# Optimization experiments

Measured on AMD Instinct MI355X. Metric: run time of the kernel, lower is better.

Reference implementation:

```python
import jax, jax.numpy as jnp
import numpy as np

EPS = 1e-12  # tf.linalg.l2_normalize epsilon

def l2norm(x, axis):
    sq = jnp.sum(x * x, axis=axis, keepdims=True)
    return x * jax.lax.rsqrt(jnp.maximum(sq, EPS))

def setup_inputs() -> dict:
    key = jax.random.key(0)
    k1, k2, k3, k4 = jax.random.split(key, 4)
    B, S, D = 32, 2048, 1024
    X = jax.random.normal(k1, (B, S, D), dtype=jnp.float32)
    lengths = jax.random.randint(k2, (B,), 1, S + 1).astype(jnp.int32)
    W_global = jax.random.normal(k3, (D, D), dtype=jnp.float32) / np.sqrt(D)
    W_local = jax.random.normal(k4, (D, D), dtype=jnp.float32) / np.sqrt(D)
    return {"X": X, "lengths": lengths, "W_global": W_global, "W_local": W_local}

def reference(X, lengths, W_global, W_local):
    B, S, D = X.shape
    # ragged -> dense with mask: token s valid iff s < lengths[b]
    mask = (jnp.arange(S)[None, :] < lengths[:, None]).astype(X.dtype)  # [B,S]
    Xm = X * mask[:, :, None]
    # global projection of sequence-sum, l2-normalized per example
    gp = l2norm(jnp.sum(Xm, axis=1) @ W_global, axis=1)  # [B,D]
    # per-token local projection, l2-normalized per token
    lp = l2norm(jnp.einsum('bsd,de->bse', Xm, W_local), axis=2)  # [B,S,D]
    # dot-product attention of local projections against global vector
    attention = jnp.einsum('bsd,bd->bs', lp, gp) * mask  # [B,S]
    # attention-weighted sum over the (ragged) sequence
    return jnp.einsum('bs,bsd->bd', attention, Xm)  # [B,D]
```

## Files before the change

### kernel.cpp

```cpp
#include <hip/hip_runtime.h>

#define NB 32
#define NS 2048
#define ND 1024

typedef unsigned short u16;
typedef unsigned int u32;
typedef __attribute__((ext_vector_type(8))) short bf16x8;
typedef __attribute__((ext_vector_type(4))) float f32x4;

__device__ __forceinline__ u16 f2bf(float f) {
    u32 u = __float_as_uint(f);
    u32 r = u + 0x7fffu + ((u >> 16) & 1u);
    return (u16)(r >> 16);
}
__device__ __forceinline__ float bf2f(u32 lo16) {
    return __uint_as_float(lo16 << 16);
}
__device__ __forceinline__ void gload_lds16(const void* g, void* l) {
    __builtin_amdgcn_global_load_lds((const __attribute__((address_space(1))) void*)g,
                                     (__attribute__((address_space(3))) void*)l, 16, 0, 0);
}

template <bool DO_STASH>
__global__ void k_prep(const float* __restrict__ X, const int* __restrict__ len,
                       float* __restrict__ sumX, u16* __restrict__ stash) {
    int b = blockIdx.x >> 5, c = blockIdx.x & 31;
    int L = len[b];
    int s0 = c * 64;
    if (s0 >= L) return;
    int n = min(64, L - s0);
    int t = threadIdx.x;
    const float4* base = (const float4*)(X + (size_t)b * NS * ND + (size_t)s0 * ND) + t;
    char* img = (char*)stash + ((size_t)blockIdx.x << 17);
    float4 acc = {0.f, 0.f, 0.f, 0.f};
    for (int i = 0; i < n; ++i) {
        float4 x = base[i * (ND / 4)];
        acc.x += x.x; acc.y += x.y; acc.z += x.z; acc.w += x.w;
        if constexpr (DO_STASH) {
            u32 lo = (u32)f2bf(x.x) | ((u32)f2bf(x.y) << 16);
            u32 hi = (u32)f2bf(x.z) | ((u32)f2bf(x.w) << 16);
            u32 off = (u32)i * 2048u + (((u32)t * 8u) ^ (((u32)(i & 7)) << 4));
            *(uint2*)(img + off) = make_uint2(lo, hi);
        }
    }
    if constexpr (DO_STASH) {
        for (int i = n; i < 64; ++i) {
            u32 off = (u32)i * 2048u + (((u32)t * 8u) ^ (((u32)(i & 7)) << 4));
            *(uint2*)(img + off) = make_uint2(0u, 0u);
        }
    }
    float* o = sumX + b * ND + t * 4;
    atomicAdd(o + 0, acc.x); atomicAdd(o + 1, acc.y);
    atomicAdd(o + 2, acc.z); atomicAdd(o + 3, acc.w);
}

__global__ void k_pack(const float* __restrict__ Wl, u16* __restrict__ pack) {
    int t = threadIdx.x;
    int f = blockIdx.x * 4 + (t >> 6);
    int lane = t & 63;
    int ks = f & 3, kc = (f >> 2) & 7, j = (f >> 5) & 3, nc = f >> 7;
    int n = nc * 64 + j * 16 + (lane & 15);
    int k0 = kc * 128 + ks * 32 + ((lane >> 4) << 3);
    u16 tmp[8];
    #pragma unroll
    for (int e = 0; e < 8; ++e)
        tmp[e] = f2bf(Wl[(size_t)(k0 + e) * ND + n]);
    *(uint4*)(pack + (size_t)f * 512 + lane * 8) = *(const uint4*)tmp;
}

__global__ void k_gproj(const float* __restrict__ sumX, const float* __restrict__ Wg,
                        float* __restrict__ yg) {
    __shared__ float sx[32][64];
    int t = threadIdx.x;
    int eb = blockIdx.x & 15, db = blockIdx.x >> 4;
    int e = eb * 64 + (t & 63);
    int bg = t >> 6;
    float acc[8] = {0.f,0.f,0.f,0.f,0.f,0.f,0.f,0.f};
    for (int d0 = db * 128; d0 < db * 128 + 128; d0 += 64) {
        __syncthreads();
        #pragma unroll
        for (int j = 0; j < 8; ++j) {
            int idx = t + j * 256;
            sx[idx >> 6][idx & 63] = sumX[(idx >> 6) * ND + d0 + (idx & 63)];
        }
        __syncthreads();
        for (int dd = 0; dd < 64; ++dd) {
            float wv = Wg[(size_t)(d0 + dd) * ND + e];
            #pragma unroll
            for (int j = 0; j < 8; ++j) acc[j] += wv * sx[bg * 8 + j][dd];
        }
    }
    #pragma unroll
    for (int j = 0; j < 8; ++j) atomicAdd(&yg[(bg * 8 + j) * ND + e], acc[j]);
}

__global__ void k_gnorm(const float* __restrict__ yg, float* __restrict__ gp) {
    int b = blockIdx.x, t = threadIdx.x;
    float4 y = ((const float4*)(yg + (size_t)b * ND))[t];
    float ss = y.x * y.x + y.y * y.y + y.z * y.z + y.w * y.w;
    #pragma unroll
    for (int o = 32; o; o >>= 1) ss += __shfl_down(ss, o);
    __shared__ float wsum[4];
    if ((t & 63) == 0) wsum[t >> 6] = ss;
    __syncthreads();
    float tot = wsum[0] + wsum[1] + wsum[2] + wsum[3];
    float sc = 1.f / sqrtf(fmaxf(tot, 1e-12f));
    float4 g = {y.x * sc, y.y * sc, y.z * sc, y.w * sc};
    ((float4*)(gp + (size_t)b * ND))[t] = g;
}

template <bool STASH>
__global__ __launch_bounds__(256, 1) void k_main(
    const float* __restrict__ X, const int* __restrict__ len,
    const u16* __restrict__ stash, const u16* __restrict__ pack,
    const float* __restrict__ gp, float* __restrict__ out) {
    __shared__ u16 Xs[64 * 1024];
    __shared__ float gp_s[1024];
    __shared__ float norm2_s[4][64];
    __shared__ float dot_s[4][64];
    __shared__ float att_s[64];

    int b = blockIdx.x >> 5;
    int tile = blockIdx.x & 31;
    int L = len[b];
    int s0 = tile * 64;
    if (s0 >= L) return;
    int valid = min(64, L - s0);
    int t = threadIdx.x;
    int lane = t & 63, w = t >> 6;

    if constexpr (STASH) {
        const char* gsrc = (const char*)stash + ((size_t)blockIdx.x << 17)
                         + (size_t)w * 32768 + (size_t)lane * 16;
        char* ldst = (char*)Xs + w * 32768;
        #pragma unroll
        for (int i = 0; i < 32; ++i)
            gload_lds16(gsrc + i * 1024, ldst + i * 1024);
    } else {
        const float* Xb = X + (size_t)b * NS * ND + (size_t)s0 * ND;
        for (int i = 0; i < 64; ++i) {
            float4 x = {0.f, 0.f, 0.f, 0.f};
            if (i < valid) x = ((const float4*)(Xb + (size_t)i * ND))[t];
            u32 lo = (u32)f2bf(x.x) | ((u32)f2bf(x.y) << 16);
            u32 hi = (u32)f2bf(x.z) | ((u32)f2bf(x.w) << 16);
            u32 off = (u32)i * 2048u + (((u32)t * 8u) ^ (((u32)(i & 7)) << 4));
            *(uint2*)((char*)Xs + off) = make_uint2(lo, hi);
        }
    }
    for (int jj = t; jj < 1024; jj += 256) gp_s[jj] = gp[b * ND + jj];
    ((float*)norm2_s)[t] = 0.f;
    ((float*)dot_s)[t] = 0.f;
    __syncthreads();

    for (int q = 0; q < 4; ++q) {
        int nc = w + q * 4;
        const u16* pb = pack + (size_t)nc * 128 * 512;
        f32x4 acc[4][4];
        #pragma unroll
        for (int rb = 0; rb < 4; ++rb)
            #pragma unroll
            for (int j = 0; j < 4; ++j) acc[rb][j] = (f32x4){0.f, 0.f, 0.f, 0.f};

        #pragma unroll 2
        for (int kc = 0; kc < 8; ++kc) {
            #pragma unroll
            for (int ks = 0; ks < 4; ++ks) {
                int kbyte = kc * 256 + ks * 64 + ((lane >> 4) << 4);
                bf16x8 a[4];
                #pragma unroll
                for (int rb = 0; rb < 4; ++rb) {
                    int row = (rb << 4) + (lane & 15);
                    a[rb] = *(const bf16x8*)((const char*)Xs + row * 2048 +
                                             (kbyte ^ ((row & 7) << 4)));
                }
                #pragma unroll
                for (int j = 0; j < 4; ++j) {
                    bf16x8 bb = *(const bf16x8*)(pb + ((size_t)(j * 32 + kc * 4 + ks)) * 512 + lane * 8);
                    #pragma unroll
                    for (int rb = 0; rb < 4; ++rb)
                        acc[rb][j] = __builtin_amdgcn_mfma_f32_16x16x32_bf16(a[rb], bb, acc[rb][j], 0, 0, 0);
                }
            }
        }
        float gpv[4];
        #pragma unroll
        for (int j = 0; j < 4; ++j) gpv[j] = gp_s[nc * 64 + j * 16 + (lane & 15)];
        #pragma unroll
        for (int rb = 0; rb < 4; ++rb) {
            #pragma unroll
            for (int reg = 0; reg < 4; ++reg) {
                float s = 0.f, d = 0.f;
                #pragma unroll
                for (int j = 0; j < 4; ++j) {
                    float y = acc[rb][j][reg];
                    s += y * y;
                    d += y * gpv[j];
                }
                s += __shfl_xor(s, 1); d += __shfl_xor(d, 1);
                s += __shfl_xor(s, 2); d += __shfl_xor(d, 2);
                s += __shfl_xor(s, 4); d += __shfl_xor(d, 4);
                s += __shfl_xor(s, 8); d += __shfl_xor(d, 8);
                if ((lane & 15) == 0) {
                    int row = (rb << 4) + ((lane >> 4) << 2) + reg;
                    norm2_s[w][row] += s;
                    dot_s[w][row] += d;
                }
            }
        }
    }
    __syncthreads();

    if (t < 64) {
        float n2 = norm2_s[0][t] + norm2_s[1][t] + norm2_s[2][t] + norm2_s[3][t];
        float dp = dot_s[0][t] + dot_s[1][t] + dot_s[2][t] + dot_s[3][t];
        att_s[t] = dp / sqrtf(fmaxf(n2, 1e-12f));
    }
    __syncthreads();

    {
        float4 acc4 = {0.f, 0.f, 0.f, 0.f};
        for (int i = 0; i < valid; ++i) {
            float a = att_s[i];
            u32 off = (u32)i * 2048u + (((u32)t * 8u) ^ (((u32)(i & 7)) << 4));
            uint2 raw = *(const uint2*)((const char*)Xs + off);
            acc4.x += a * bf2f(raw.x & 0xffffu);
            acc4.y += a * __uint_as_float(raw.x & 0xffff0000u);
            acc4.z += a * bf2f(raw.y & 0xffffu);
            acc4.w += a * __uint_as_float(raw.y & 0xffff0000u);
        }
        float* o = out + b * ND + t * 4;
        atomicAdd(o + 0, acc4.x); atomicAdd(o + 1, acc4.y);
        atomicAdd(o + 2, acc4.z); atomicAdd(o + 3, acc4.w);
    }
}

extern "C" void kernel_launch(void* const* d_in, const int* in_sizes, int n_in,
                              void* d_out, int out_size, void* d_ws, size_t ws_size,
                              hipStream_t stream) {
    (void)in_sizes; (void)n_in; (void)out_size;
    const float* X  = (const float*)d_in[0];
    const int* len  = (const int*)d_in[1];
    const float* Wg = (const float*)d_in[2];
    const float* Wl = (const float*)d_in[3];
    float* out = (float*)d_out;

    char* ws = (char*)d_ws;
    float* sumX = (float*)(ws + 0);
    float* yg   = (float*)(ws + 131072);
    float* gp   = (float*)(ws + 262144);
    u16*   pack = (u16*)(ws + 393216);
    u16*   stash= (u16*)(ws + 2490368);
    const size_t need = 2490368ull + (size_t)NB * 32 * 131072ull;
    int use_stash = ws_size >= need;

    hipMemsetAsync(sumX, 0, 2 * NB * ND * sizeof(float), stream);
    hipMemsetAsync(out, 0, NB * ND * sizeof(float), stream);

    if (use_stash)
        k_prep<true> <<<NB * 32, 256, 0, stream>>>(X, len, sumX, stash);
    else
        k_prep<false><<<NB * 32, 256, 0, stream>>>(X, len, sumX, stash);
    k_pack <<<512, 256, 0, stream>>>(Wl, pack);
    k_gproj<<<128, 256, 0, stream>>>(sumX, Wg, yg);
    k_gnorm<<<NB, 256, 0, stream>>>(yg, gp);
    if (use_stash)
        k_main<true> <<<NB * 32, 256, 0, stream>>>(X, len, stash, pack, gp, out);
    else
        k_main<false><<<NB * 32, 256, 0, stream>>>(X, len, stash, pack, gp, out);
}
```

Baseline: 727.6 us.

## Drop LDS X tile; read MFMA-fragment-packed stash directly from global

The stash and the packed W_local are rewritten into per-fragment layouts, so each MFMA operand becomes one contiguous 16-byte global load per lane, and the 128KB LDS tile of X is removed. Without that LDS allocation the launch bound is raised to 3 blocks per CU for more occupancy. The final attention-weighted sum now reads fp32 X from global instead of the bf16 LDS copy. This makes the result more exact but rereads X from memory. The trade is less LDS traffic and more occupancy against relying on L2/global bandwidth for A and B operand reuse across the four waves.

```diff
diff --git a/kernel.cpp b/kernel.cpp
--- a/kernel.cpp
+++ b/kernel.cpp
@@ -13,13 +13,6 @@
     u32 u = __float_as_uint(f);
     u32 r = u + 0x7fffu + ((u >> 16) & 1u);
     return (u16)(r >> 16);
-}
-__device__ __forceinline__ float bf2f(u32 lo16) {
-    return __uint_as_float(lo16 << 16);
-}
-__device__ __forceinline__ void gload_lds16(const void* g, void* l) {
-    __builtin_amdgcn_global_load_lds((const __attribute__((address_space(1))) void*)g,
-                                     (__attribute__((address_space(3))) void*)l, 16, 0, 0);
 }
 
 template <bool DO_STASH>
@@ -32,7 +25,8 @@
     int n = min(64, L - s0);
     int t = threadIdx.x;
     const float4* base = (const float4*)(X + (size_t)b * NS * ND + (size_t)s0 * ND) + t;
-    char* img = (char*)stash + ((size_t)blockIdx.x << 17);
+    u16* tb = stash + ((size_t)blockIdx.x << 16)
+            + (size_t)(t >> 3) * 2048 + (((t >> 1) & 3) << 7) + ((t & 1) << 2);
     float4 acc = {0.f, 0.f, 0.f, 0.f};
     for (int i = 0; i < n; ++i) {
         float4 x = base[i * (ND / 4)];
@@ -40,15 +34,12 @@
         if constexpr (DO_STASH) {
             u32 lo = (u32)f2bf(x.x) | ((u32)f2bf(x.y) << 16);
             u32 hi = (u32)f2bf(x.z) | ((u32)f2bf(x.w) << 16);
-            u32 off = (u32)i * 2048u + (((u32)t * 8u) ^ (((u32)(i & 7)) << 4));
-            *(uint2*)(img + off) = make_uint2(lo, hi);
+            *(uint2*)(tb + (i >> 4) * 512 + (i & 15) * 8) = make_uint2(lo, hi);
         }
     }
     if constexpr (DO_STASH) {
-        for (int i = n; i < 64; ++i) {
-            u32 off = (u32)i * 2048u + (((u32)t * 8u) ^ (((u32)(i & 7)) << 4));
-            *(uint2*)(img + off) = make_uint2(0u, 0u);
-        }
+        for (int i = n; i < 64; ++i)
+            *(uint2*)(tb + (i >> 4) * 512 + (i & 15) * 8) = make_uint2(0u, 0u);
     }
     float* o = sumX + b * ND + t * 4;
     atomicAdd(o + 0, acc.x); atomicAdd(o + 1, acc.y);
@@ -59,9 +50,9 @@
     int t = threadIdx.x;
     int f = blockIdx.x * 4 + (t >> 6);
     int lane = t & 63;
-    int ks = f & 3, kc = (f >> 2) & 7, j = (f >> 5) & 3, nc = f >> 7;
+    int j = f & 3, kk = (f >> 2) & 31, nc = f >> 7;
     int n = nc * 64 + j * 16 + (lane & 15);
-    int k0 = kc * 128 + ks * 32 + ((lane >> 4) << 3);
+    int k0 = kk * 32 + ((lane >> 4) << 3);
     u16 tmp[8];
     #pragma unroll
     for (int e = 0; e < 8; ++e)
@@ -111,11 +102,10 @@
 }
 
 template <bool STASH>
-__global__ __launch_bounds__(256, 1) void k_main(
+__global__ __launch_bounds__(256, 3) void k_main(
     const float* __restrict__ X, const int* __restrict__ len,
     const u16* __restrict__ stash, const u16* __restrict__ pack,
     const float* __restrict__ gp, float* __restrict__ out) {
-    __shared__ u16 Xs[64 * 1024];
     __shared__ float gp_s[1024];
     __shared__ float norm2_s[4][64];
     __shared__ float dot_s[4][64];
@@ -130,32 +120,17 @@
     int t = threadIdx.x;
     int lane = t & 63, w = t >> 6;
 
-    if constexpr (STASH) {
-        const char* gsrc = (const char*)stash + ((size_t)blockIdx.x << 17)
-                         + (size_t)w * 32768 + (size_t)lane * 16;
-        char* ldst = (char*)Xs + w * 32768;
-        #pragma unroll
-        for (int i = 0; i < 32; ++i)
-            gload_lds16(gsrc + i * 1024, ldst + i * 1024);
-    } else {
-        const float* Xb = X + (size_t)b * NS * ND + (size_t)s0 * ND;
-        for (int i = 0; i < 64; ++i) {
-            float4 x = {0.f, 0.f, 0.f, 0.f};
-            if (i < valid) x = ((const float4*)(Xb + (size_t)i * ND))[t];
-            u32 lo = (u32)f2bf(x.x) | ((u32)f2bf(x.y) << 16);
-            u32 hi = (u32)f2bf(x.z) | ((u32)f2bf(x.w) << 16);
-            u32 off = (u32)i * 2048u + (((u32)t * 8u) ^ (((u32)(i & 7)) << 4));
-            *(uint2*)((char*)Xs + off) = make_uint2(lo, hi);
-        }
-    }
     for (int jj = t; jj < 1024; jj += 256) gp_s[jj] = gp[b * ND + jj];
     ((float*)norm2_s)[t] = 0.f;
     ((float*)dot_s)[t] = 0.f;
     __syncthreads();
 
+    const u16* ta = stash + ((size_t)blockIdx.x << 16) + lane * 8;
+    const float* Xb = X + (size_t)b * NS * ND + (size_t)s0 * ND;
+
     for (int q = 0; q < 4; ++q) {
         int nc = w + q * 4;
-        const u16* pb = pack + (size_t)nc * 128 * 512;
+        const u16* pb = pack + (size_t)nc * 65536 + lane * 8;
         f32x4 acc[4][4];
         #pragma unroll
         for (int rb = 0; rb < 4; ++rb)
@@ -163,25 +138,37 @@
             for (int j = 0; j < 4; ++j) acc[rb][j] = (f32x4){0.f, 0.f, 0.f, 0.f};
 
         #pragma unroll 2
-        for (int kc = 0; kc < 8; ++kc) {
-            #pragma unroll
-            for (int ks = 0; ks < 4; ++ks) {
-                int kbyte = kc * 256 + ks * 64 + ((lane >> 4) << 4);
-                bf16x8 a[4];
+        for (int kk = 0; kk < 32; ++kk) {
+            bf16x8 a[4], bb[4];
+            if constexpr (STASH) {
+                #pragma unroll
+                for (int rb = 0; rb < 4; ++rb)
+                    a[rb] = *(const bf16x8*)(ta + (kk * 4 + rb) * 512);
+            } else {
+                int kb = kk * 32 + ((lane >> 4) << 3);
                 #pragma unroll
                 for (int rb = 0; rb < 4; ++rb) {
                     int row = (rb << 4) + (lane & 15);
-                    a[rb] = *(const bf16x8*)((const char*)Xs + row * 2048 +
-                                             (kbyte ^ ((row & 7) << 4)));
-                }
-                #pragma unroll
-                for (int j = 0; j < 4; ++j) {
-                    bf16x8 bb = *(const bf16x8*)(pb + ((size_t)(j * 32 + kc * 4 + ks)) * 512 + lane * 8);
-                    #pragma unroll
-                    for (int rb = 0; rb < 4; ++rb)
-                        acc[rb][j] = __builtin_amdgcn_mfma_f32_16x16x32_bf16(a[rb], bb, acc[rb][j], 0, 0, 0);
+                    bf16x8 av = {0,0,0,0,0,0,0,0};
+                    if (row < valid) {
+                        float4 x0 = *(const float4*)(Xb + (size_t)row * ND + kb);
+                        float4 x1 = *(const float4*)(Xb + (size_t)row * ND + kb + 4);
+                        av[0] = (short)f2bf(x0.x); av[1] = (short)f2bf(x0.y);
+                        av[2] = (short)f2bf(x0.z); av[3] = (short)f2bf(x0.w);
+                        av[4] = (short)f2bf(x1.x); av[5] = (short)f2bf(x1.y);
+                        av[6] = (short)f2bf(x1.z); av[7] = (short)f2bf(x1.w);
+                    }
+                    a[rb] = av;
                 }
             }
+            #pragma unroll
+            for (int j = 0; j < 4; ++j)
+                bb[j] = *(const bf16x8*)(pb + (kk * 4 + j) * 512);
+            #pragma unroll
+            for (int j = 0; j < 4; ++j)
+                #pragma unroll
+                for (int rb = 0; rb < 4; ++rb)
+                    acc[rb][j] = __builtin_amdgcn_mfma_f32_16x16x32_bf16(a[rb], bb[j], acc[rb][j], 0, 0, 0);
         }
         float gpv[4];
         #pragma unroll
@@ -220,14 +207,11 @@
 
     {
         float4 acc4 = {0.f, 0.f, 0.f, 0.f};
+        #pragma unroll 4
         for (int i = 0; i < valid; ++i) {
             float a = att_s[i];
-            u32 off = (u32)i * 2048u + (((u32)t * 8u) ^ (((u32)(i & 7)) << 4));
-            uint2 raw = *(const uint2*)((const char*)Xs + off);
-            acc4.x += a * bf2f(raw.x & 0xffffu);
-            acc4.y += a * __uint_as_float(raw.x & 0xffff0000u);
-            acc4.z += a * bf2f(raw.y & 0xffffu);
-            acc4.w += a * __uint_as_float(raw.y & 0xffff0000u);
+            float4 x = ((const float4*)(Xb + (size_t)i * ND))[t];
+            acc4.x += a * x.x; acc4.y += a * x.y; acc4.z += a * x.z; acc4.w += a * x.w;
         }
         float* o = out + b * ND + t * 4;
         atomicAdd(o + 0, acc4.x); atomicAdd(o + 1, acc4.y);
```

Result: faster. 605.0 us (-16.9%).
